# Performance work log

Measured on AMD Instinct MI355X. Metric: run time of the kernel, lower is better.

The kernel has to match this reference:

```python
import jax, jax.numpy as jnp
import numpy as np

N_HEADS = 16
N_EMBED = 1024
HEAD = N_EMBED // N_HEADS
NEG = -1e10


def setup_inputs() -> dict:
    key = jax.random.key(0)
    ks = jax.random.split(key, 12)
    B, Tq, Tk, C = 4, 2048, 2048, N_EMBED
    s = 1.0 / np.sqrt(C)
    return {
        "x": jax.random.normal(ks[0], (B, Tq, C), jnp.float32),
        "features": jax.random.normal(ks[1], (B, Tk, C), jnp.float32),
        "mask": jax.random.randint(ks[2], (B, 1, 1, Tk), 0, 2, jnp.int32),
        "wq": jax.random.normal(ks[3], (C, C), jnp.float32) * s,
        "bq": jnp.zeros((C,), jnp.float32),
        "wk": jax.random.normal(ks[4], (C, C), jnp.float32) * s,
        "bk": jnp.zeros((C,), jnp.float32),
        "wv": jax.random.normal(ks[5], (C, C), jnp.float32) * s,
        "bv": jnp.zeros((C,), jnp.float32),
        "wo": jax.random.normal(ks[6], (C, C), jnp.float32) * s,
        "bo": jnp.zeros((C,), jnp.float32),
    }


def reference(x, features, mask, wq, bq, wk, bk, wv, bv, wo, bo):
    B, Tq, C = x.shape
    Tk = features.shape[1]
    # project and split heads: [B, H, T, Dh]
    q = (x @ wq + bq).reshape(B, Tq, N_HEADS, HEAD).transpose(0, 2, 1, 3)
    k = (features @ wk + bk).reshape(B, Tk, N_HEADS, HEAD).transpose(0, 2, 1, 3)
    v = (features @ wv + bv).reshape(B, Tk, N_HEADS, HEAD).transpose(0, 2, 1, 3)
    attn = jnp.einsum("bhqd,bhkd->bhqk", q, k) / np.sqrt(HEAD)
    attn = jnp.where(mask == 0, NEG, attn)
    attn = jax.nn.softmax(attn, axis=-1)  # dropout p=0 (eval)
    out = jnp.einsum("bhqk,bhkd->bhqd", attn, v)
    out = out.transpose(0, 2, 1, 3).reshape(B, Tq, C)
    return out @ wo + bo
```

## Files before the change

kernel.cpp:

```cpp
#include <hip/hip_runtime.h>
#include <stdint.h>

typedef __attribute__((ext_vector_type(8))) short bf16x8;
typedef __attribute__((ext_vector_type(4))) float f32x4;
typedef __attribute__((ext_vector_type(16))) float f32x16;

#define BB 4
#define NH 16
#define TT 2048
#define HD 64
#define CC 1024

__device__ __forceinline__ unsigned short f2bf(float f) {
  unsigned int u = __builtin_bit_cast(unsigned int, f);
  u += 0x7fff + ((u >> 16) & 1);
  return (unsigned short)(u >> 16);
}

__device__ __forceinline__ float fast_exp2(float x) {
#if __has_builtin(__builtin_amdgcn_exp2f)
  return __builtin_amdgcn_exp2f(x);
#else
  return exp2f(x);
#endif
}

__device__ __forceinline__ unsigned int cvtpk(float lo, float hi) {
  unsigned int r;
  asm("v_cvt_pk_bf16_f32 %0, %1, %2" : "=v"(r) : "v"(lo), "v"(hi));
  return r;
}

__device__ __forceinline__ void plswap(unsigned int& a, unsigned int& b) {
#if __has_builtin(__builtin_amdgcn_permlane32_swap)
  auto r = __builtin_amdgcn_permlane32_swap(a, b, false, false);
  a = r[0];
  b = r[1];
#else
  unsigned int as = __shfl_xor((int)a, 32), bs = __shfl_xor((int)b, 32);
  bool hi = (threadIdx.x & 32) != 0;
  unsigned int na = hi ? bs : a;
  unsigned int nb = hi ? b : as;
  a = na; b = nb;
#endif
}

__device__ __forceinline__ void g2l16(const void* g, void* s) {
  __builtin_amdgcn_global_load_lds(
      (const __attribute__((address_space(1))) unsigned int*)g,
      (__attribute__((address_space(3))) unsigned int*)s, 16, 0, 0);
}

__global__ __launch_bounds__(256) void cast2(
    const float* __restrict__ x, const float* __restrict__ ft,
    unsigned short* __restrict__ xb, unsigned short* __restrict__ fb, int n) {
  const float* in = blockIdx.y ? ft : x;
  unsigned short* out = blockIdx.y ? fb : xb;
  int i = (blockIdx.x * 256 + threadIdx.x) * 4;
  if (i >= n) return;
  float4 v = *(const float4*)(in + i);
  ushort4 o;
  o.x = f2bf(v.x); o.y = f2bf(v.y); o.z = f2bf(v.z); o.w = f2bf(v.w);
  *(ushort4*)(out + i) = o;
}

__global__ __launch_bounds__(256) void make_fmask(
    const int* __restrict__ mask, float* __restrict__ fm, int n) {
  int i = blockIdx.x * 256 + threadIdx.x;
  if (i < n) fm[i] = mask[i] ? 0.f : -1.44269504e10f;
}

__global__ __launch_bounds__(256) void transpose_cast_w4(
    const float* __restrict__ wq, const float* __restrict__ wk,
    const float* __restrict__ wv, const float* __restrict__ wo,
    unsigned short* __restrict__ wqkvt, unsigned short* __restrict__ wot) {
  __shared__ float tile[32][33];
  const int z = blockIdx.z;
  const float* w = (z == 0) ? wq : (z == 1) ? wk : (z == 2) ? wv : wo;
  unsigned short* wt = (z < 3) ? wqkvt + (size_t)z * CC * CC : wot;
  int nb = blockIdx.x * 32, kb = blockIdx.y * 32;
  int tx = threadIdx.x, ty = threadIdx.y;
#pragma unroll
  for (int r = ty; r < 32; r += 8)
    tile[r][tx] = w[(size_t)(kb + r) * CC + nb + tx];
  __syncthreads();
#pragma unroll
  for (int r = ty; r < 32; r += 8)
    wt[(size_t)(nb + r) * CC + kb + tx] = f2bf(tile[tx][r]);
}

__global__ __launch_bounds__(256) void gemm_qkv(
    const unsigned short* __restrict__ xb, const unsigned short* __restrict__ fb,
    const unsigned short* __restrict__ Wt,
    const float* __restrict__ bq, const float* __restrict__ bk,
    const float* __restrict__ bv,
    unsigned short* __restrict__ Qb, unsigned short* __restrict__ Kb,
    unsigned short* __restrict__ Vtb, float qscale) {
  __shared__ unsigned short As[128 * 32];
  __shared__ unsigned short Bs[128 * 32];
  int lin = blockIdx.y * gridDim.x + blockIdx.x;
  int cpx = (gridDim.x * gridDim.y) >> 3;
  int sw = (lin & 7) * cpx + (lin >> 3);
  const int n0g = (sw % 24) * 128;
  const int m0 = (sw / 24) * 128;
  const int sec = n0g >> 10;
  const int n0 = n0g & (CC - 1);
  const unsigned short* A = (sec == 0) ? xb : fb;
  const unsigned short* Bt = Wt + (size_t)n0g * CC;

  const int t = threadIdx.x, l = t & 63, w = t >> 6;
  const int lr = l & 15, lg = l >> 4;
  const int wr = w >> 1, wc = w & 1;
  f32x4 acc[4][4] = {};
  for (int k0 = 0; k0 < CC; k0 += 32) {
#pragma unroll
    for (int i = 0; i < 2; ++i) {
      int c = w * 64 + l + i * 256;
      int row = c >> 2, cb = (c & 3) * 8;
      g2l16(A + (size_t)(m0 + row) * CC + k0 + cb, (char*)As + c * 16);
      g2l16(Bt + (size_t)row * CC + k0 + cb, (char*)Bs + c * 16);
    }
    __syncthreads();
    bf16x8 af[4], bfr[4];
#pragma unroll
    for (int mi = 0; mi < 4; ++mi)
      af[mi] = *(const bf16x8*)(As + (wr * 64 + mi * 16 + lr) * 32 + lg * 8);
#pragma unroll
    for (int nj = 0; nj < 4; ++nj)
      bfr[nj] = *(const bf16x8*)(Bs + (wc * 64 + nj * 16 + lr) * 32 + lg * 8);
#pragma unroll
    for (int mi = 0; mi < 4; ++mi)
#pragma unroll
      for (int nj = 0; nj < 4; ++nj)
        acc[mi][nj] = __builtin_amdgcn_mfma_f32_16x16x32_bf16(
            af[mi], bfr[nj], acc[mi][nj], 0, 0, 0);
    __syncthreads();
  }
  const float* bp = (sec == 0) ? bq : (sec == 1) ? bk : bv;
  const float scale = (sec == 0) ? qscale : 1.0f;
#pragma unroll
  for (int mi = 0; mi < 4; ++mi) {
#pragma unroll
    for (int nj = 0; nj < 4; ++nj) {
      int col = n0 + wc * 64 + nj * 16 + lr;
      float bias = bp[col];
#pragma unroll
      for (int j = 0; j < 4; ++j) {
        int rowm = m0 + wr * 64 + mi * 16 + lg * 4 + j;
        float v = (acc[mi][nj][j] + bias) * scale;
        int b_ = rowm >> 11, tq = rowm & (TT - 1);
        int h_ = col >> 6, d_ = col & (HD - 1);
        if (sec < 2) {
          unsigned short* dst = (sec == 0) ? Qb : Kb;
          dst[((size_t)((b_ * NH + h_) * TT + tq) << 6) + d_] = f2bf(v);
        } else {
          Vtb[((size_t)((b_ * NH + h_) * HD + d_) * TT) + tq] = f2bf(v);
        }
      }
    }
  }
}

__global__ __launch_bounds__(256) void gemm_out(
    const unsigned short* __restrict__ A, const unsigned short* __restrict__ Bt,
    const float* __restrict__ bias, float* __restrict__ Out) {
  __shared__ unsigned short As[128 * 32];
  __shared__ unsigned short Bs[128 * 32];
  int lin = blockIdx.y * gridDim.x + blockIdx.x;
  int cpx = (gridDim.x * gridDim.y) >> 3;
  int sw = (lin & 7) * cpx + (lin >> 3);
  const int n0 = (sw % 8) * 128;
  const int m0 = (sw / 8) * 128;
  const int t = threadIdx.x, l = t & 63, w = t >> 6;
  const int lr = l & 15, lg = l >> 4;
  const int wr = w >> 1, wc = w & 1;
  f32x4 acc[4][4] = {};
  for (int k0 = 0; k0 < CC; k0 += 32) {
#pragma unroll
    for (int i = 0; i < 2; ++i) {
      int c = w * 64 + l + i * 256;
      int row = c >> 2, cb = (c & 3) * 8;
      g2l16(A + (size_t)(m0 + row) * CC + k0 + cb, (char*)As + c * 16);
      g2l16(Bt + (size_t)(n0 + row) * CC + k0 + cb, (char*)Bs + c * 16);
    }
    __syncthreads();
    bf16x8 af[4], bfr[4];
#pragma unroll
    for (int mi = 0; mi < 4; ++mi)
      af[mi] = *(const bf16x8*)(As + (wr * 64 + mi * 16 + lr) * 32 + lg * 8);
#pragma unroll
    for (int nj = 0; nj < 4; ++nj)
      bfr[nj] = *(const bf16x8*)(Bs + (wc * 64 + nj * 16 + lr) * 32 + lg * 8);
#pragma unroll
    for (int mi = 0; mi < 4; ++mi)
#pragma unroll
      for (int nj = 0; nj < 4; ++nj)
        acc[mi][nj] = __builtin_amdgcn_mfma_f32_16x16x32_bf16(
            af[mi], bfr[nj], acc[mi][nj], 0, 0, 0);
    __syncthreads();
  }
#pragma unroll
  for (int mi = 0; mi < 4; ++mi) {
#pragma unroll
    for (int nj = 0; nj < 4; ++nj) {
      int col = n0 + wc * 64 + nj * 16 + lr;
      float bv = bias[col];
#pragma unroll
      for (int j = 0; j < 4; ++j) {
        int rowm = m0 + wr * 64 + mi * 16 + lg * 4 + j;
        Out[(size_t)rowm * CC + col] = acc[mi][nj][j] + bv;
      }
    }
  }
}

__device__ __forceinline__ void stage_tile(
    int t, int kb, const unsigned short* __restrict__ Kg,
    const unsigned short* __restrict__ Vg,
    unsigned short* Kd, unsigned short* Vd) {
#pragma unroll
  for (int i = 0; i < 2; ++i) {
    int s = t + i * 256;
    int row = s >> 3, cb = (s & 7) * 16;
    int csw = cb ^ ((row & 7) << 4);
    g2l16(Kg + (size_t)(kb + row) * HD + (csw >> 1), (char*)Kd + s * 16);
    g2l16(Vg + (size_t)row * TT + kb + (csw >> 1), (char*)Vd + s * 16);
  }
}

__global__ __launch_bounds__(256) void attn_fwd5(
    const unsigned short* __restrict__ Q, const unsigned short* __restrict__ K,
    const unsigned short* __restrict__ Vt, const float* __restrict__ fm,
    unsigned short* __restrict__ O) {
  __shared__ unsigned short Kl[2][64 * 64];
  __shared__ unsigned short Vl[2][64 * 64];
  __shared__ float fml[TT];
  const int t = threadIdx.x, l = t & 63, w = t >> 6;
  const int q5 = l & 31, hi = l >> 5;
  int lin = blockIdx.y * gridDim.x + blockIdx.x;
  int sw = (lin & 7) * 128 + (lin >> 3);
  const int bx = sw & 15, bh = sw >> 4;
  const int b_ = bh >> 4, h_ = bh & (NH - 1);
  const int q = bx * 128 + w * 32 + q5;
  const size_t base = (size_t)bh * TT * HD;
  const unsigned short* Kg = K + base;
  const unsigned short* Vg = Vt + (size_t)bh * HD * TT;

  bf16x8 qf[4];
  {
    const unsigned short* qp = Q + base + (size_t)q * HD + 8 * hi;
#pragma unroll
    for (int dk = 0; dk < 4; ++dk) qf[dk] = *(const bf16x8*)(qp + dk * 16);
  }
  f32x16 ot[2];
#pragma unroll
  for (int i = 0; i < 16; ++i) { ot[0][i] = 0.f; ot[1][i] = 0.f; }
  float m_ = -3.0e38f, l_ = 0.f;

  {
    const float* fmg = fm + b_ * TT;
#pragma unroll
    for (int i = 0; i < 2; ++i) {
      int s = t + i * 256;
      g2l16(fmg + s * 4, (char*)fml + s * 16);
    }
  }
  stage_tile(t, 0, Kg, Vg, Kl[0], Vl[0]);
  asm volatile("s_waitcnt vmcnt(0)" ::: "memory");
  __syncthreads();

  int cur = 0;
  for (int kt = 0; kt < TT / 64; ++kt) {
    const int kb = kt * 64;
    if (kt < TT / 64 - 1) stage_tile(t, kb + 64, Kg, Vg, Kl[cur ^ 1], Vl[cur ^ 1]);

    f32x16 s[2];
#pragma unroll
    for (int kk = 0; kk < 2; ++kk) {
#pragma unroll
      for (int g = 0; g < 4; ++g) {
        float4 mv = *(const float4*)(fml + kb + kk * 32 + g * 8 + 4 * hi);
        s[kk][4 * g + 0] = mv.x; s[kk][4 * g + 1] = mv.y;
        s[kk][4 * g + 2] = mv.z; s[kk][4 * g + 3] = mv.w;
      }
    }
    __builtin_amdgcn_s_setprio(1);
#pragma unroll
    for (int kk = 0; kk < 2; ++kk) {
      const int row = kk * 32 + q5;
      const char* krow = (const char*)Kl[cur] + row * 128;
      const int swz = (row & 7) << 4;
#pragma unroll
      for (int dk = 0; dk < 4; ++dk) {
        bf16x8 kf = *(const bf16x8*)(krow + ((dk * 32 + hi * 16) ^ swz));
        s[kk] = __builtin_amdgcn_mfma_f32_32x32x16_bf16(kf, qf[dk], s[kk], 0, 0, 0);
      }
    }
    __builtin_amdgcn_s_setprio(0);

    float t0 = fmaxf(s[0][0], s[0][1]);
    float t1 = fmaxf(s[0][2], s[0][3]);
#pragma unroll
    for (int i = 4; i < 16; i += 4) {
      t0 = fmaxf(t0, fmaxf(s[0][i + 0], s[0][i + 1]));
      t1 = fmaxf(t1, fmaxf(s[0][i + 2], s[0][i + 3]));
    }
#pragma unroll
    for (int i = 0; i < 16; i += 4) {
      t0 = fmaxf(t0, fmaxf(s[1][i + 0], s[1][i + 1]));
      t1 = fmaxf(t1, fmaxf(s[1][i + 2], s[1][i + 3]));
    }
    float tm = fmaxf(t0, t1);
    tm = fmaxf(tm, __shfl_xor(tm, 32));
    const bool resc = !__all(tm <= m_ + 8.f);
    const float nm = resc ? fmaxf(m_, tm) : m_;
    float p0 = 0.f, p1 = 0.f, p2 = 0.f, p3 = 0.f;
#pragma unroll
    for (int kk = 0; kk < 2; ++kk)
#pragma unroll
      for (int i = 0; i < 16; i += 4) {
        float e0 = fast_exp2(s[kk][i + 0] - nm);
        float e1 = fast_exp2(s[kk][i + 1] - nm);
        float e2 = fast_exp2(s[kk][i + 2] - nm);
        float e3 = fast_exp2(s[kk][i + 3] - nm);
        s[kk][i + 0] = e0; s[kk][i + 1] = e1;
        s[kk][i + 2] = e2; s[kk][i + 3] = e3;
        p0 += e0; p1 += e1; p2 += e2; p3 += e3;
      }
    float ps = (p0 + p1) + (p2 + p3);
    if (resc) {
      float r = fast_exp2(m_ - nm);
      l_ = l_ * r + ps;
#pragma unroll
      for (int i = 0; i < 16; ++i) { ot[0][i] *= r; ot[1][i] *= r; }
      m_ = nm;
    } else {
      l_ += ps;
    }

    unsigned int wl[2][4], wh[2][4];
#pragma unroll
    for (int kk = 0; kk < 2; ++kk)
#pragma unroll
      for (int g = 0; g < 4; ++g) {
        wl[kk][g] = cvtpk(s[kk][4 * g + 0], s[kk][4 * g + 1]);
        wh[kk][g] = cvtpk(s[kk][4 * g + 2], s[kk][4 * g + 3]);
      }
    bf16x8 pa[4];
#pragma unroll
    for (int ks = 0; ks < 4; ++ks) {
      const int kk = ks >> 1, gA = 2 * (ks & 1), gB = gA + 1;
      unsigned int a0 = wl[kk][gA], b0 = wl[kk][gB];
      unsigned int a1 = wh[kk][gA], b1 = wh[kk][gB];
      plswap(a0, b0);
      plswap(a1, b1);
      unsigned int pw[4] = {a0, a1, b0, b1};
      pa[ks] = *(bf16x8*)pw;
    }

    __builtin_amdgcn_s_setprio(1);
#pragma unroll
    for (int dt = 0; dt < 2; ++dt) {
      const int row = dt * 32 + q5;
      const char* vrow = (const char*)Vl[cur] + row * 128;
      const int swz = (row & 7) << 4;
#pragma unroll
      for (int ks = 0; ks < 4; ++ks) {
        bf16x8 vf = *(const bf16x8*)(vrow + ((ks * 32 + hi * 16) ^ swz));
        ot[dt] = __builtin_amdgcn_mfma_f32_32x32x16_bf16(vf, pa[ks], ot[dt], 0, 0, 0);
      }
    }
    __builtin_amdgcn_s_setprio(0);

    asm volatile("s_waitcnt vmcnt(0)" ::: "memory");
    __syncthreads();
    cur ^= 1;
  }

  float l_tot = l_ + __shfl_xor(l_, 32);
  const float inv = 1.f / l_tot;
  unsigned short* orow = O + ((size_t)(b_ * TT) + q) * CC + h_ * 64 + 4 * hi;
#pragma unroll
  for (int dt = 0; dt < 2; ++dt)
#pragma unroll
    for (int g = 0; g < 4; ++g) {
      unsigned short pk4[4];
#pragma unroll
      for (int j = 0; j < 4; ++j) pk4[j] = f2bf(ot[dt][4 * g + j] * inv);
      *(ushort4*)(orow + dt * 32 + 8 * g) = *(ushort4*)pk4;
    }
}

extern "C" void kernel_launch(void* const* d_in, const int* in_sizes, int n_in,
                              void* d_out, int out_size, void* d_ws, size_t ws_size,
                              hipStream_t stream) {
  const float* x  = (const float*)d_in[0];
  const float* ft = (const float*)d_in[1];
  const int* mask = (const int*)d_in[2];
  const float* wq = (const float*)d_in[3];
  const float* bq = (const float*)d_in[4];
  const float* wk = (const float*)d_in[5];
  const float* bk = (const float*)d_in[6];
  const float* wv = (const float*)d_in[7];
  const float* bv = (const float*)d_in[8];
  const float* wo = (const float*)d_in[9];
  const float* bo = (const float*)d_in[10];
  float* out = (float*)d_out;

  char* ws = (char*)d_ws;
  const size_t NTOK = (size_t)BB * TT;
  const size_t SB = NTOK * CC * 2;
  unsigned short* xb   = (unsigned short*)ws; ws += SB;
  unsigned short* fb   = (unsigned short*)ws; ws += SB;
  unsigned short* Qb   = (unsigned short*)ws; ws += SB;
  unsigned short* Kb   = (unsigned short*)ws; ws += SB;
  unsigned short* Vtb  = (unsigned short*)ws; ws += SB;
  unsigned short* AO   = (unsigned short*)ws; ws += SB;
  unsigned short* wqkvt = (unsigned short*)ws; ws += (size_t)3 * CC * CC * 2;
  unsigned short* wot   = (unsigned short*)ws; ws += (size_t)CC * CC * 2;
  float* fmk = (float*)ws; ws += NTOK * 4;

  int ncast = (int)(NTOK * CC);
  dim3 gc(ncast / 4 / 256, 2);
  cast2<<<gc, 256, 0, stream>>>(x, ft, xb, fb, ncast);
  dim3 tb(32, 8), tg(32, 32, 4);
  transpose_cast_w4<<<tg, tb, 0, stream>>>(wq, wk, wv, wo, wqkvt, wot);
  make_fmask<<<(int)(NTOK / 256), 256, 0, stream>>>(mask, fmk, (int)NTOK);

  const float qscale = 0.125f * 1.44269504f;
  dim3 gq(24, 64);
  gemm_qkv<<<gq, 256, 0, stream>>>(xb, fb, wqkvt, bq, bk, bv, Qb, Kb, Vtb, qscale);

  dim3 ga(16, 64);
  attn_fwd5<<<ga, 256, 0, stream>>>(Qb, Kb, Vtb, fmk, AO);

  dim3 go(8, 64);
  gemm_out<<<go, 256, 0, stream>>>(AO, wot, bo, out);
}
```

Baseline: 258.0 us.

## Unroll attention K/V double buffer by two with precomputed LDS offsets

The attention loop is manually unrolled by two, so each buffer offset becomes a compile-time constant. Per-lane LDS read addresses and global staging pointers are precomputed once and advanced by pointer increments, which removes per-iteration swizzle and address math. The mask is now read straight from global memory instead of being staged in LDS, shrinking LDS to 32KB, which may allow more blocks per CU. The cost is extra global/L2 traffic for mask loads and more live registers for the precomputed offsets.

```diff
diff --git a/kernel.cpp b/kernel.cpp
--- a/kernel.cpp
+++ b/kernel.cpp
@@ -1,5 +1,6 @@
 #include <hip/hip_runtime.h>
 #include <stdint.h>
+#include <type_traits>
 
 typedef __attribute__((ext_vector_type(8))) short bf16x8;
 typedef __attribute__((ext_vector_type(4))) float f32x4;
@@ -214,27 +215,11 @@
   }
 }
 
-__device__ __forceinline__ void stage_tile(
-    int t, int kb, const unsigned short* __restrict__ Kg,
-    const unsigned short* __restrict__ Vg,
-    unsigned short* Kd, unsigned short* Vd) {
-#pragma unroll
-  for (int i = 0; i < 2; ++i) {
-    int s = t + i * 256;
-    int row = s >> 3, cb = (s & 7) * 16;
-    int csw = cb ^ ((row & 7) << 4);
-    g2l16(Kg + (size_t)(kb + row) * HD + (csw >> 1), (char*)Kd + s * 16);
-    g2l16(Vg + (size_t)row * TT + kb + (csw >> 1), (char*)Vd + s * 16);
-  }
-}
-
-__global__ __launch_bounds__(256) void attn_fwd5(
+__global__ __launch_bounds__(256) void attn_fwd6(
     const unsigned short* __restrict__ Q, const unsigned short* __restrict__ K,
     const unsigned short* __restrict__ Vt, const float* __restrict__ fm,
     unsigned short* __restrict__ O) {
-  __shared__ unsigned short Kl[2][64 * 64];
-  __shared__ unsigned short Vl[2][64 * 64];
-  __shared__ float fml[TT];
+  __shared__ __attribute__((aligned(64))) char ldsb[32768];
   const int t = threadIdx.x, l = t & 63, w = t >> 6;
   const int q5 = l & 31, hi = l >> 5;
   int lin = blockIdx.y * gridDim.x + blockIdx.x;
@@ -252,50 +237,70 @@
 #pragma unroll
     for (int dk = 0; dk < 4; ++dk) qf[dk] = *(const bf16x8*)(qp + dk * 16);
   }
+
+  int ka[2][4], va[2][4];
+#pragma unroll
+  for (int kk = 0; kk < 2; ++kk) {
+    int row = kk * 32 + q5, swz = (row & 7) << 4;
+#pragma unroll
+    for (int dk = 0; dk < 4; ++dk)
+      ka[kk][dk] = row * 128 + ((dk * 32 + hi * 16) ^ swz);
+  }
+#pragma unroll
+  for (int dt = 0; dt < 2; ++dt) {
+    int row = dt * 32 + q5, swz = (row & 7) << 4;
+#pragma unroll
+    for (int ks = 0; ks < 4; ++ks)
+      va[dt][ks] = row * 128 + ((ks * 32 + hi * 16) ^ swz);
+  }
+
+  const int s1 = t + 256;
+  const int r0 = t >> 3, c0 = (t & 7) * 16, x0 = c0 ^ ((r0 & 7) << 4);
+  const int r1 = s1 >> 3, c1 = (s1 & 7) * 16, x1 = c1 ^ ((r1 & 7) << 4);
+  const unsigned short* gk0 = Kg + r0 * HD + (x0 >> 1);
+  const unsigned short* gk1 = Kg + r1 * HD + (x1 >> 1);
+  const unsigned short* gv0 = Vg + (size_t)r0 * TT + (x0 >> 1);
+  const unsigned short* gv1 = Vg + (size_t)r1 * TT + (x1 >> 1);
+  const float4* mp4 = (const float4*)(fm + (size_t)b_ * TT) + hi;
+
+  auto stage = [&](int boff) {
+    g2l16(gk0, ldsb + t * 16 + boff);
+    g2l16(gk1, ldsb + t * 16 + 4096 + boff);
+    g2l16(gv0, ldsb + 16384 + t * 16 + boff);
+    g2l16(gv1, ldsb + 16384 + t * 16 + 4096 + boff);
+    gk0 += 4096; gk1 += 4096; gv0 += 64; gv1 += 64;
+  };
+
   f32x16 ot[2];
 #pragma unroll
   for (int i = 0; i < 16; ++i) { ot[0][i] = 0.f; ot[1][i] = 0.f; }
   float m_ = -3.0e38f, l_ = 0.f;
 
-  {
-    const float* fmg = fm + b_ * TT;
-#pragma unroll
-    for (int i = 0; i < 2; ++i) {
-      int s = t + i * 256;
-      g2l16(fmg + s * 4, (char*)fml + s * 16);
-    }
-  }
-  stage_tile(t, 0, Kg, Vg, Kl[0], Vl[0]);
+  stage(0);
   asm volatile("s_waitcnt vmcnt(0)" ::: "memory");
   __syncthreads();
 
-  int cur = 0;
-  for (int kt = 0; kt < TT / 64; ++kt) {
-    const int kb = kt * 64;
-    if (kt < TT / 64 - 1) stage_tile(t, kb + 64, Kg, Vg, Kl[cur ^ 1], Vl[cur ^ 1]);
-
+  auto compute = [&](auto Bc) {
+    constexpr int BO = decltype(Bc)::value;
     f32x16 s[2];
 #pragma unroll
-    for (int kk = 0; kk < 2; ++kk) {
+    for (int kk = 0; kk < 2; ++kk)
 #pragma unroll
       for (int g = 0; g < 4; ++g) {
-        float4 mv = *(const float4*)(fml + kb + kk * 32 + g * 8 + 4 * hi);
+        float4 mv = mp4[kk * 8 + g * 2];
         s[kk][4 * g + 0] = mv.x; s[kk][4 * g + 1] = mv.y;
         s[kk][4 * g + 2] = mv.z; s[kk][4 * g + 3] = mv.w;
       }
-    }
+    mp4 += 16;
+
     __builtin_amdgcn_s_setprio(1);
 #pragma unroll
-    for (int kk = 0; kk < 2; ++kk) {
-      const int row = kk * 32 + q5;
-      const char* krow = (const char*)Kl[cur] + row * 128;
-      const int swz = (row & 7) << 4;
+    for (int kk = 0; kk < 2; ++kk)
 #pragma unroll
       for (int dk = 0; dk < 4; ++dk) {
-        bf16x8 kf = *(const bf16x8*)(krow + ((dk * 32 + hi * 16) ^ swz));
+        bf16x8 kf = *(const bf16x8*)(ldsb + ka[kk][dk] + BO);
         s[kk] = __builtin_amdgcn_mfma_f32_32x32x16_bf16(kf, qf[dk], s[kk], 0, 0, 0);
       }
-    }
     __builtin_amdgcn_s_setprio(0);
 
     float t0 = fmaxf(s[0][0], s[0][1]);
@@ -360,21 +365,24 @@
 
     __builtin_amdgcn_s_setprio(1);
 #pragma unroll
-    for (int dt = 0; dt < 2; ++dt) {
-      const int row = dt * 32 + q5;
-      const char* vrow = (const char*)Vl[cur] + row * 128;
-      const int swz = (row & 7) << 4;
+    for (int dt = 0; dt < 2; ++dt)
 #pragma unroll
       for (int ks = 0; ks < 4; ++ks) {
-        bf16x8 vf = *(const bf16x8*)(vrow + ((ks * 32 + hi * 16) ^ swz));
+        bf16x8 vf = *(const bf16x8*)(ldsb + 16384 + va[dt][ks] + BO);
         ot[dt] = __builtin_amdgcn_mfma_f32_32x32x16_bf16(vf, pa[ks], ot[dt], 0, 0, 0);
       }
-    }
     __builtin_amdgcn_s_setprio(0);
-
+  };
+
+  for (int j = 0; j < 16; ++j) {
+    stage(8192);
+    compute(std::integral_constant<int, 0>{});
     asm volatile("s_waitcnt vmcnt(0)" ::: "memory");
     __syncthreads();
-    cur ^= 1;
+    if (j < 15) stage(0);
+    compute(std::integral_constant<int, 8192>{});
+    asm volatile("s_waitcnt vmcnt(0)" ::: "memory");
+    __syncthreads();
   }
 
   float l_tot = l_ + __shfl_xor(l_, 32);
@@ -432,7 +440,7 @@
   gemm_qkv<<<gq, 256, 0, stream>>>(xb, fb, wqkvt, bq, bk, bv, Qb, Kb, Vtb, qscale);
 
   dim3 ga(16, 64);
-  attn_fwd5<<<ga, 256, 0, stream>>>(Qb, Kb, Vtb, fmk, AO);
+  attn_fwd6<<<ga, 256, 0, stream>>>(Qb, Kb, Vtb, fmk, AO);
 
   dim3 go(8, 64);
   gemm_out<<<go, 256, 0, stream>>>(AO, wot, bo, out);
```

New measurement: 252.8 us. -2.0%, faster.
